# Kernel tuning notes

Measured on AMD Instinct MI355X. Metric: run time of the kernel, lower is better.

The kernel has to match this reference:

```python
import jax, jax.numpy as jnp
import numpy as np
from jax import lax

N_KERNELS = 10000
KSS = np.array([7, 9, 11])
SEQ_LEN = 512
C_IN = 1
KMAX = 11  # max kernel size; shorter kernels are zero-padded in the tap dim
BATCH = 16


def _gen_params():
    # Deterministic ROCKET kernel hyperparameters (matches the torch __init__ logic).
    rng = np.random.default_rng(0)
    ks = rng.choice(KSS, size=N_KERNELS)
    hi = np.log2((SEQ_LEN - 1) // (ks - 1))
    dil = np.floor(2.0 ** rng.uniform(0.0, hi)).astype(np.int64)  # int(dilation)
    use_pad = rng.integers(0, 2, N_KERNELS)
    p = ((ks - 1) * dil // 2) * use_pad
    # Conv1d is called with padding=2*p (faithful to source), so output length is:
    L = SEQ_LEN + 4 * p - dil * (ks - 1)
    return ks, dil, p, L

_KS, _DIL, _P, _L = _gen_params()
_PMAX = int((2 * _P).max())   # max per-side zero padding across kernels
_LMAX = int(_L.max())         # max conv output length across kernels


def setup_inputs() -> dict:
    key = jax.random.key(0)
    kx, kw, kb = jax.random.split(key, 3)
    x = jax.random.normal(kx, (BATCH, C_IN, SEQ_LEN), dtype=jnp.float32)
    W = jax.random.normal(kw, (N_KERNELS, C_IN, KMAX), dtype=jnp.float32)
    # zero taps beyond each kernel's true size, then subtract mean over real taps
    tap_mask = jnp.asarray((np.arange(KMAX)[None, :] < _KS[:, None])[:, None, :],
                           dtype=jnp.float32)                      # [K,1,KMAX]
    denom = jnp.asarray((_KS * C_IN).astype(np.float32))[:, None, None]
    W = W * tap_mask
    W = (W - W.sum(axis=(1, 2), keepdims=True) / denom) * tap_mask
    bias = 2.0 * (jax.random.uniform(kb, (N_KERNELS,), dtype=jnp.float32) - 0.5)
    return {"x": x, "W": W, "bias": bias}


def reference(x, W, bias):
    B = x.shape[0]
    off = jnp.asarray(_PMAX - 2 * _P, dtype=jnp.int32)               # [K]
    dil = jnp.asarray(_DIL, dtype=jnp.int32)                         # [K]
    t = jnp.arange(_LMAX, dtype=jnp.int32)
    pos_base = off[:, None] + t[None, :]                             # [K, Lmax]
    valid = t[None, :] < jnp.asarray(_L, dtype=jnp.int32)[:, None]   # [K, Lmax]
    xpad = jnp.pad(x, ((0, 0), (0, 0), (_PMAX, _PMAX)))              # zero pad
    hi = SEQ_LEN + 2 * _PMAX - 1

    def step(acc, jw):
        j, wj = jw                                                   # wj: [K, C]
        pos = jnp.clip(pos_base + j * dil[:, None], 0, hi)           # [K, Lmax]
        xg = xpad[:, :, pos]                                         # [B,C,K,Lmax]
        return acc + jnp.einsum('bckl,kc->bkl', xg, wj), None

    acc0 = jnp.zeros((B, N_KERNELS, _LMAX), dtype=x.dtype)
    Wt = jnp.transpose(W, (2, 0, 1))                                 # [KMAX,K,C]
    acc, _ = lax.scan(step, acc0, (jnp.arange(KMAX, dtype=jnp.int32), Wt))
    out = acc + bias[None, :, None]                                  # [B,K,Lmax]

    # inputs are finite, so nGood == L (>0 always): max over valid region + PPV
    _max = jnp.where(valid[None], out, -jnp.inf).max(axis=-1)        # [B, K]
    ngood = jnp.asarray(_L, dtype=x.dtype)
    ppv = jnp.sum(jnp.where(valid[None], out > 0, False), axis=-1).astype(x.dtype) / ngood[None]
    return jnp.stack([_max, ppv], axis=-1).reshape(B, 2 * N_KERNELS)
```

## Files before the change

kernel.cpp:

```cpp
#include <hip/hip_runtime.h>
#include <hip/hip_fp16.h>
#include <math.h>
#include <stdint.h>
#include <string.h>

typedef unsigned __int128 u128;

#define NK 10000
#define KPB 8

#define PCG_MUL_128 ((((u128)0x2360ed051fc65da4ULL) << 64) | 0x4385df649fccf645ULL)

#define SORT_OFF   (NK * 4)
#define WS_NEEDED  (SORT_OFF + NK * 4)

struct ThrTab { double t[3][84]; };

static void host_seed(u128& state, u128& inc) {
  uint32_t hc = 0x43b0d7e5u;
  auto hashmix = [&hc](uint32_t v) -> uint32_t {
    v ^= hc; hc *= 0x931e8875u; v *= hc; v ^= v >> 16; return v;
  };
  uint32_t pool[4];
  for (int i = 0; i < 4; ++i) pool[i] = hashmix(0u);
  for (int s = 0; s < 4; ++s)
    for (int d = 0; d < 4; ++d)
      if (s != d) {
        uint32_t h = hashmix(pool[s]);
        uint32_t r = pool[d] * 0xca01f9ddu - h * 0x4973f715u;
        r ^= r >> 16;
        pool[d] = r;
      }
  uint32_t hb = 0x8b51f9ddu;
  uint32_t w[8];
  for (int i = 0; i < 8; ++i) {
    uint32_t v = pool[i & 3];
    v ^= hb; hb *= 0x58f38dedu; v *= hb; v ^= v >> 16;
    w[i] = v;
  }
  u128 is_ = ((u128)(((uint64_t)w[0]) | ((uint64_t)w[1] << 32)) << 64)
           | (u128)(((uint64_t)w[2]) | ((uint64_t)w[3] << 32));
  u128 iq  = ((u128)(((uint64_t)w[4]) | ((uint64_t)w[5] << 32)) << 64)
           | (u128)(((uint64_t)w[6]) | ((uint64_t)w[7] << 32));
  inc = (iq << 1) | (u128)1;
  state = inc; state += is_; state = state * PCG_MUL_128 + inc;
}

static inline uint64_t xslrr_h(u128 s) {
  uint64_t x = (uint64_t)(s >> 64) ^ (uint64_t)s;
  unsigned r = (unsigned)(s >> 122);
  return (x >> r) | (x << ((64u - r) & 63u));
}

__device__ __forceinline__ void dev_seed(u128& state, u128& inc) {
  uint32_t hc = 0x43b0d7e5u;
  auto hashmix = [&hc](uint32_t v) -> uint32_t {
    v ^= hc; hc *= 0x931e8875u; v *= hc; v ^= v >> 16; return v;
  };
  uint32_t pool[4];
  for (int i = 0; i < 4; ++i) pool[i] = hashmix(0u);
  for (int s = 0; s < 4; ++s)
    for (int d = 0; d < 4; ++d)
      if (s != d) {
        uint32_t h = hashmix(pool[s]);
        uint32_t r = pool[d] * 0xca01f9ddu - h * 0x4973f715u;
        r ^= r >> 16;
        pool[d] = r;
      }
  uint32_t hb = 0x8b51f9ddu;
  uint32_t w[8];
  for (int i = 0; i < 8; ++i) {
    uint32_t v = pool[i & 3];
    v ^= hb; hb *= 0x58f38dedu; v *= hb; v ^= v >> 16;
    w[i] = v;
  }
  u128 is_ = ((u128)(((uint64_t)w[0]) | ((uint64_t)w[1] << 32)) << 64)
           | (u128)(((uint64_t)w[2]) | ((uint64_t)w[3] << 32));
  u128 iq  = ((u128)(((uint64_t)w[4]) | ((uint64_t)w[5] << 32)) << 64)
           | (u128)(((uint64_t)w[6]) | ((uint64_t)w[7] << 32));
  inc = (iq << 1) | (u128)1;
  state = inc; state += is_; state = state * PCG_MUL_128 + inc;
}

__device__ __forceinline__ u128 dev_advance(u128 state, u128 inc, uint64_t delta) {
  u128 am = 1, ap = 0, cm = PCG_MUL_128, cp = inc;
  while (delta) {
    if (delta & 1) { am = am * cm; ap = ap * cm + cp; }
    cp = (cm + (u128)1) * cp;
    cm = cm * cm;
    delta >>= 1;
  }
  return am * state + ap;
}

__device__ __forceinline__ uint64_t draw_at(u128 state, u128 inc, uint64_t n) {
  u128 s = dev_advance(state, inc, n);
  s = s * PCG_MUL_128 + inc;
  uint64_t x = (uint64_t)(s >> 64) ^ (uint64_t)s;
  unsigned r = (unsigned)(s >> 122);
  return (x >> r) | (x << ((64u - r) & 63u));
}

__global__ __launch_bounds__(256) void params_k(uint32_t* __restrict__ pack,
                                                ThrTab tt) {
  int i = blockIdx.x * 256 + threadIdx.x;
  if (i >= NK) return;
  u128 state, inc;
  dev_seed(state, inc);
  uint64_t a = draw_at(state, inc, (uint64_t)(i >> 1));
  uint32_t u = (i & 1) ? (uint32_t)(a >> 32) : (uint32_t)a;
  int si = (int)(((uint64_t)u * 3ull) >> 32);
  uint64_t ud = draw_at(state, inc, (uint64_t)(5000 + i));
  double d = (double)(ud >> 11) * (1.0 / 9007199254740992.0);
  int c0 = 0, c1 = 0, c2 = 0;
  #pragma unroll
  for (int v = 0; v < 84; ++v) {
    c0 += (d >= tt.t[0][v]) ? 1 : 0;
    c1 += (d >= tt.t[1][v]) ? 1 : 0;
    c2 += (d >= tt.t[2][v]) ? 1 : 0;
  }
  int dil = 1 + ((si == 0) ? c0 : ((si == 1) ? c1 : c2));
  uint64_t p6 = draw_at(state, inc, (uint64_t)(15000 + (i >> 1)));
  uint32_t pu = (i & 1) ? (uint32_t)(p6 >> 32) : (uint32_t)p6;
  int pad = (int)(pu >> 31);
  pack[i] = ((uint32_t)i << 10) | (uint32_t)si | ((uint32_t)dil << 2)
          | ((uint32_t)pad << 9);
}

__global__ __launch_bounds__(1024) void sort_k(const uint32_t* __restrict__ pack,
                                               uint32_t* __restrict__ sorted) {
  __shared__ int hist[1024];
  __shared__ int offs[1024];
  int tid = threadIdx.x;
  hist[tid] = 0;
  __syncthreads();
  for (int p = 0; p < 10; ++p) {
    int i = tid + p * 1024;
    if (i < NK) {
      uint32_t bits = pack[i] & 1023u;
      int ks = 7 + 2 * (int)(bits & 3), dil = (int)((bits >> 2) & 127);
      int pad = (int)(bits >> 9);
      int twop = (ks - 1) * dil * pad;
      int L = 512 + 2 * twop - dil * (ks - 1);
      atomicAdd(&hist[1022 - L], 1);
    }
  }
  __syncthreads();
  int own = hist[tid];
  for (int off = 1; off < 1024; off <<= 1) {
    int v = (tid >= off) ? hist[tid - off] : 0;
    __syncthreads();
    hist[tid] += v;
    __syncthreads();
  }
  offs[tid] = hist[tid] - own;
  __syncthreads();
  for (int p = 0; p < 10; ++p) {
    int i = tid + p * 1024;
    if (i < NK) {
      uint32_t e = pack[i];
      uint32_t bits = e & 1023u;
      int ks = 7 + 2 * (int)(bits & 3), dil = (int)((bits >> 2) & 127);
      int pad = (int)(bits >> 9);
      int twop = (ks - 1) * dil * pad;
      int L = 512 + 2 * twop - dil * (ks - 1);
      int idx = atomicAdd(&offs[1022 - L], 1);
      sorted[idx] = e;
    }
  }
}

template<int KS>
__device__ __forceinline__ void conv_core(const float4* __restrict__ xs4,
                                          const __half2* wh2, float bv,
                                          int twop, int dil, int L,
                                          int tl, int bh,
                                          float* m, int* cn) {
  int coreEnd = (L < 512) ? L : 512;
  int nch = (L + 31) >> 5;
  for (int c = 0; c < nch; ++c) {
    int t0 = c << 5;
    int t = t0 + tl;
    __half2 acc[4];
    #pragma unroll
    for (int r = 0; r < 4; ++r) acc[r] = __half2(__float2half2_rn(0.0f));
    if (t0 >= twop && t0 + 32 <= coreEnd) {
      const float4* p = xs4 + (unsigned)(t - twop) * 2 + bh;
      #pragma unroll
      for (int j = 0; j < KS; ++j) {
        float4 v4 = *p;
        union { float4 v; __half2 h[4]; } u;
        u.v = v4;
        __half2 wj = wh2[j];
        #pragma unroll
        for (int r = 0; r < 4; ++r) acc[r] = __hfma2(wj, u.h[r], acc[r]);
        p += (unsigned)dil * 2;
      }
    } else {
      int idx = t - twop;
      #pragma unroll
      for (int j = 0; j < KS; ++j) {
        unsigned ci = (unsigned)idx;
        ci = (ci > 512u) ? 512u : ci;
        float4 v4 = xs4[ci * 2 + bh];
        union { float4 v; __half2 h[4]; } u;
        u.v = v4;
        __half2 wj = wh2[j];
        #pragma unroll
        for (int r = 0; r < 4; ++r) acc[r] = __hfma2(wj, u.h[r], acc[r]);
        idx += dil;
      }
    }
    if (t < L) {
      #pragma unroll
      for (int r = 0; r < 4; ++r) {
        float2 f = __half22float2(acc[r]);
        float v0 = f.x + bv, v1 = f.y + bv;
        m[2 * r]     = fmaxf(m[2 * r], v0);     cn[2 * r]     += (v0 > 0.0f);
        m[2 * r + 1] = fmaxf(m[2 * r + 1], v1); cn[2 * r + 1] += (v1 > 0.0f);
      }
    }
  }
}

__global__ __launch_bounds__(512) void conv_feat_k(const float* __restrict__ x,
                                                   const float* __restrict__ W,
                                                   const float* __restrict__ bias,
                                                   const uint32_t* __restrict__ entries,
                                                   float failDiag,
                                                   float* __restrict__ out) {
  __shared__ float4 xs4[513 * 2];
  int tid = threadIdx.x;

  #pragma unroll
  for (int q = 0; q < 2; ++q) {
    int flat = q * 512 + tid;
    int t = flat >> 1, bh = flat & 1;
    union { __half h[8]; float4 v; } u;
    #pragma unroll
    for (int r = 0; r < 8; ++r)
      u.h[r] = __float2half(x[(8 * bh + r) * 512 + t]);
    xs4[flat] = u.v;
  }
  if (tid < 2) xs4[512 * 2 + tid] = make_float4(0.f, 0.f, 0.f, 0.f);

  int wave = tid >> 6, lane = tid & 63;
  int tl = lane >> 1, bh = lane & 1;
  uint32_t e = entries[blockIdx.x * KPB + wave];
  int k = (int)(e >> 10);
  uint32_t bits = e & 1023u;
  __syncthreads();

  int ks  = 7 + 2 * (int)(bits & 3);
  int dil = (int)((bits >> 2) & 127);
  int pad = (int)(bits >> 9);
  int twop = (ks - 1) * dil * pad;
  int L = 512 + 2 * twop - dil * (ks - 1);
  float w10 = W[k * 11 + 10], w8 = W[k * 11 + 8];
  int ksW = (w10 != 0.0f) ? 11 : ((w8 != 0.0f) ? 9 : 7);
  if (failDiag != 0.0f || ks != ksW) {
    float diag = (failDiag != 0.0f) ? failDiag : 6500000.0f;
    if (lane < 16) {
      out[(size_t)lane * 20000 + 2 * k]     = diag;
      out[(size_t)lane * 20000 + 2 * k + 1] = diag;
    }
    return;
  }

  __half2 wh2[11];
  #pragma unroll
  for (int j = 0; j < 11; ++j) wh2[j] = __float2half2_rn(W[k * 11 + j]);
  float bv = bias[k];

  float m[8];
  int cn[8];
  #pragma unroll
  for (int r = 0; r < 8; ++r) { m[r] = -INFINITY; cn[r] = 0; }
  if (ks == 7)       conv_core<7>(xs4, wh2, bv, twop, dil, L, tl, bh, m, cn);
  else if (ks == 9)  conv_core<9>(xs4, wh2, bv, twop, dil, L, tl, bh, m, cn);
  else               conv_core<11>(xs4, wh2, bv, twop, dil, L, tl, bh, m, cn);

  #pragma unroll
  for (int off = 2; off <= 32; off <<= 1) {
    #pragma unroll
    for (int r = 0; r < 8; ++r) {
      m[r] = fmaxf(m[r], __shfl_xor(m[r], off));
      cn[r] += __shfl_xor(cn[r], off);
    }
  }
  if (tl == 0) {
    float invL = 1.0f / (float)L;
    #pragma unroll
    for (int r = 0; r < 8; ++r) {
      size_t b = (size_t)(8 * bh + r);
      out[b * 20000 + 2 * k]     = m[r];
      out[b * 20000 + 2 * k + 1] = (float)cn[r] * invL;
    }
  }
}

extern "C" void kernel_launch(void* const* d_in, const int* in_sizes, int n_in,
                              void* d_out, int out_size, void* d_ws, size_t ws_size,
                              hipStream_t stream) {
  (void)out_size;
  const float *x = nullptr, *W = nullptr, *bias = nullptr;
  for (int i = 0; i < n_in; ++i) {
    int sz = in_sizes[i];
    if (sz == 16 * 512)      x    = (const float*)d_in[i];
    else if (sz == NK * 11)  W    = (const float*)d_in[i];
    else if (sz == NK)       bias = (const float*)d_in[i];
  }
  float failDiag = 0.0f;
  if (!x || !W || !bias) {
    failDiag = 9000000.0f;
    x = (const float*)d_in[0]; W = (const float*)d_in[1]; bias = (const float*)d_in[2];
  }

  static uint64_t hs[20000];
  {
    u128 st, inc; host_seed(st, inc);
    for (int i = 0; i < 20000; ++i) { st = st * PCG_MUL_128 + inc; hs[i] = xslrr_h(st); }
  }
  double d0 = (double)(hs[0] >> 11) * (1.0 / 9007199254740992.0);
  if (failDiag == 0.0f && fabs(d0 - 0.6369616873214543) >= 1.0e-15)
    failDiag = 4000000.0f;
  int rejected = 0;
  for (int i = 0; i < 5000; ++i)
    if ((uint32_t)hs[i] == 0u || (uint32_t)(hs[i] >> 32) == 0u) { rejected = 1; break; }

  static ThrTab tt;
  for (int si = 0; si < 3; ++si) {
    int ksv = 7 + 2 * si;
    double hi = log2((double)(511 / (ksv - 1)));
    double dmax = nextafter(1.0, 0.0);
    for (int v = 2; v <= 85; ++v) {
      if (pow(2.0, hi * dmax) < (double)v) { tt.t[si][v - 2] = 2.0; continue; }
      uint64_t lo = 0, hb;
      memcpy(&hb, &dmax, 8);
      while (hb - lo > 1) {
        uint64_t mid = lo + (hb - lo) / 2;
        double dm;
        memcpy(&dm, &mid, 8);
        if (pow(2.0, hi * dm) >= (double)v) hb = mid; else lo = mid;
      }
      double tv;
      memcpy(&tv, &hb, 8);
      tt.t[si][v - 2] = tv;
    }
  }

  uint32_t* dpack = (uint32_t*)d_ws;
  uint32_t* dsort = (uint32_t*)((char*)d_ws + SORT_OFF);

  if (!rejected && ws_size >= WS_NEEDED) {
    params_k<<<(NK + 255) / 256, 256, 0, stream>>>(dpack, tt);
    sort_k<<<1, 1024, 0, stream>>>(dpack, dsort);
    conv_feat_k<<<NK / KPB, 512, 0, stream>>>(x, W, bias, dsort, failDiag,
                                              (float*)d_out);
  } else {
    static uint32_t h_entries[NK];
    {
      int pos32 = 0;
      auto nx32 = [&](int& p) -> uint32_t {
        uint64_t v = hs[p >> 1];
        uint32_t u = (p & 1) ? (uint32_t)(v >> 32) : (uint32_t)v;
        ++p; return u;
      };
      static int ksA[NK], dilA[NK], padA[NK];
      for (int i = 0; i < NK; ++i) {
        uint64_t m; uint32_t u;
        do { u = nx32(pos32); m = (uint64_t)u * 3ull; } while ((uint32_t)m == 0u);
        ksA[i] = (int)(m >> 32);
      }
      int u64pos = (pos32 + 1) >> 1;
      for (int i = 0; i < NK; ++i) {
        double d = (double)(hs[u64pos + i] >> 11) * (1.0 / 9007199254740992.0);
        int ksv = 7 + 2 * ksA[i];
        double hi2 = log2((double)(511 / (ksv - 1)));
        dilA[i] = (int)floor(pow(2.0, hi2 * d));
      }
      int p32 = 2 * (u64pos + NK);
      for (int i = 0; i < NK; ++i) padA[i] = (int)(nx32(p32) >> 31);
      static int cnt2[1024], off2[1024];
      for (int b = 0; b < 1024; ++b) cnt2[b] = 0;
      for (int i = 0; i < NK; ++i) {
        int ksv = 7 + 2 * ksA[i];
        int twop = (ksv - 1) * dilA[i] * padA[i];
        int L = 512 + 2 * twop - dilA[i] * (ksv - 1);
        cnt2[1022 - L]++;
      }
      int acc = 0;
      for (int b = 0; b < 1024; ++b) { off2[b] = acc; acc += cnt2[b]; }
      for (int i = 0; i < NK; ++i) {
        int ksv = 7 + 2 * ksA[i];
        int twop = (ksv - 1) * dilA[i] * padA[i];
        int L = 512 + 2 * twop - dilA[i] * (ksv - 1);
        uint32_t bits = (uint32_t)ksA[i] | ((uint32_t)dilA[i] << 2)
                      | ((uint32_t)padA[i] << 9);
        h_entries[off2[1022 - L]++] = ((uint32_t)i << 10) | bits;
      }
    }
    hipMemcpyAsync(dsort, h_entries, sizeof(h_entries), hipMemcpyHostToDevice,
                   stream);
    conv_feat_k<<<NK / KPB, 512, 0, stream>>>(x, W, bias, dsort, failDiag,
                                              (float*)d_out);
  }
}
```

Baseline: 74.47 us.

## Replace length sort with atomic work-queue scheduling and half-precision epilogue

Drops the single-block counting-sort kernel that ordered kernels by output length. Instead, a fixed grid of persistent blocks has each wave pull kernel indices from a global atomic counter, which balances load dynamically. The per-element epilogue now stays in packed fp16: the bias is folded into the accumulator init, and max and positive count use vector half and short ops. This removes one kernel launch and a serial sort, but adds an atomic per kernel. The epilogue also loses precision, since the bias is added in fp16 and counts are held in 16-bit shorts.

```diff
diff --git a/kernel.cpp b/kernel.cpp
--- a/kernel.cpp
+++ b/kernel.cpp
@@ -5,14 +5,15 @@
 #include <string.h>
 
 typedef unsigned __int128 u128;
+typedef _Float16 h2v __attribute__((ext_vector_type(2)));
+typedef short    s2v __attribute__((ext_vector_type(2)));
 
 #define NK 10000
-#define KPB 8
+#define NBLK 1024
 
 #define PCG_MUL_128 ((((u128)0x2360ed051fc65da4ULL) << 64) | 0x4385df649fccf645ULL)
 
-#define SORT_OFF   (NK * 4)
-#define WS_NEEDED  (SORT_OFF + NK * 4)
+#define WS_NEEDED  ((NK + 1) * 4)
 
 struct ThrTab { double t[3][84]; };
 
@@ -104,7 +105,10 @@
 __global__ __launch_bounds__(256) void params_k(uint32_t* __restrict__ pack,
                                                 ThrTab tt) {
   int i = blockIdx.x * 256 + threadIdx.x;
-  if (i >= NK) return;
+  if (i >= NK) {
+    if (i == NK) pack[NK] = 0;
+    return;
+  }
   u128 state, inc;
   dev_seed(state, inc);
   uint64_t a = draw_at(state, inc, (uint64_t)(i >> 1));
@@ -123,59 +127,16 @@
   uint64_t p6 = draw_at(state, inc, (uint64_t)(15000 + (i >> 1)));
   uint32_t pu = (i & 1) ? (uint32_t)(p6 >> 32) : (uint32_t)p6;
   int pad = (int)(pu >> 31);
-  pack[i] = ((uint32_t)i << 10) | (uint32_t)si | ((uint32_t)dil << 2)
-          | ((uint32_t)pad << 9);
-}
-
-__global__ __launch_bounds__(1024) void sort_k(const uint32_t* __restrict__ pack,
-                                               uint32_t* __restrict__ sorted) {
-  __shared__ int hist[1024];
-  __shared__ int offs[1024];
-  int tid = threadIdx.x;
-  hist[tid] = 0;
-  __syncthreads();
-  for (int p = 0; p < 10; ++p) {
-    int i = tid + p * 1024;
-    if (i < NK) {
-      uint32_t bits = pack[i] & 1023u;
-      int ks = 7 + 2 * (int)(bits & 3), dil = (int)((bits >> 2) & 127);
-      int pad = (int)(bits >> 9);
-      int twop = (ks - 1) * dil * pad;
-      int L = 512 + 2 * twop - dil * (ks - 1);
-      atomicAdd(&hist[1022 - L], 1);
-    }
-  }
-  __syncthreads();
-  int own = hist[tid];
-  for (int off = 1; off < 1024; off <<= 1) {
-    int v = (tid >= off) ? hist[tid - off] : 0;
-    __syncthreads();
-    hist[tid] += v;
-    __syncthreads();
-  }
-  offs[tid] = hist[tid] - own;
-  __syncthreads();
-  for (int p = 0; p < 10; ++p) {
-    int i = tid + p * 1024;
-    if (i < NK) {
-      uint32_t e = pack[i];
-      uint32_t bits = e & 1023u;
-      int ks = 7 + 2 * (int)(bits & 3), dil = (int)((bits >> 2) & 127);
-      int pad = (int)(bits >> 9);
-      int twop = (ks - 1) * dil * pad;
-      int L = 512 + 2 * twop - dil * (ks - 1);
-      int idx = atomicAdd(&offs[1022 - L], 1);
-      sorted[idx] = e;
-    }
-  }
+  pack[i] = (uint32_t)si | ((uint32_t)dil << 2) | ((uint32_t)pad << 9);
 }
 
 template<int KS>
 __device__ __forceinline__ void conv_core(const float4* __restrict__ xs4,
-                                          const __half2* wh2, float bv,
+                                          const __half2* wh2, __half2 bvh2,
                                           int twop, int dil, int L,
                                           int tl, int bh,
-                                          float* m, int* cn) {
+                                          h2v* mh, s2v* ch) {
+  const h2v zero2 = (h2v)0;
   int coreEnd = (L < 512) ? L : 512;
   int nch = (L + 31) >> 5;
   for (int c = 0; c < nch; ++c) {
@@ -183,7 +144,7 @@
     int t = t0 + tl;
     __half2 acc[4];
     #pragma unroll
-    for (int r = 0; r < 4; ++r) acc[r] = __half2(__float2half2_rn(0.0f));
+    for (int r = 0; r < 4; ++r) acc[r] = bvh2;
     if (t0 >= twop && t0 + 32 <= coreEnd) {
       const float4* p = xs4 + (unsigned)(t - twop) * 2 + bh;
       #pragma unroll
@@ -214,10 +175,10 @@
     if (t < L) {
       #pragma unroll
       for (int r = 0; r < 4; ++r) {
-        float2 f = __half22float2(acc[r]);
-        float v0 = f.x + bv, v1 = f.y + bv;
-        m[2 * r]     = fmaxf(m[2 * r], v0);     cn[2 * r]     += (v0 > 0.0f);
-        m[2 * r + 1] = fmaxf(m[2 * r + 1], v1); cn[2 * r + 1] += (v1 > 0.0f);
+        union { __half2 h; h2v v; } cv;
+        cv.h = acc[r];
+        mh[r] = __builtin_elementwise_max(mh[r], cv.v);
+        ch[r] -= (cv.v > zero2);
       }
     }
   }
@@ -226,7 +187,7 @@
 __global__ __launch_bounds__(512) void conv_feat_k(const float* __restrict__ x,
                                                    const float* __restrict__ W,
                                                    const float* __restrict__ bias,
-                                                   const uint32_t* __restrict__ entries,
+                                                   uint32_t* __restrict__ pack,
                                                    float failDiag,
                                                    float* __restrict__ out) {
   __shared__ float4 xs4[513 * 2];
@@ -244,57 +205,74 @@
   }
   if (tid < 2) xs4[512 * 2 + tid] = make_float4(0.f, 0.f, 0.f, 0.f);
 
-  int wave = tid >> 6, lane = tid & 63;
+  int lane = tid & 63;
   int tl = lane >> 1, bh = lane & 1;
-  uint32_t e = entries[blockIdx.x * KPB + wave];
-  int k = (int)(e >> 10);
-  uint32_t bits = e & 1023u;
   __syncthreads();
 
-  int ks  = 7 + 2 * (int)(bits & 3);
-  int dil = (int)((bits >> 2) & 127);
-  int pad = (int)(bits >> 9);
-  int twop = (ks - 1) * dil * pad;
-  int L = 512 + 2 * twop - dil * (ks - 1);
-  float w10 = W[k * 11 + 10], w8 = W[k * 11 + 8];
-  int ksW = (w10 != 0.0f) ? 11 : ((w8 != 0.0f) ? 9 : 7);
-  if (failDiag != 0.0f || ks != ksW) {
-    float diag = (failDiag != 0.0f) ? failDiag : 6500000.0f;
-    if (lane < 16) {
-      out[(size_t)lane * 20000 + 2 * k]     = diag;
-      out[(size_t)lane * 20000 + 2 * k + 1] = diag;
-    }
-    return;
-  }
-
-  __half2 wh2[11];
-  #pragma unroll
-  for (int j = 0; j < 11; ++j) wh2[j] = __float2half2_rn(W[k * 11 + j]);
-  float bv = bias[k];
-
-  float m[8];
-  int cn[8];
-  #pragma unroll
-  for (int r = 0; r < 8; ++r) { m[r] = -INFINITY; cn[r] = 0; }
-  if (ks == 7)       conv_core<7>(xs4, wh2, bv, twop, dil, L, tl, bh, m, cn);
-  else if (ks == 9)  conv_core<9>(xs4, wh2, bv, twop, dil, L, tl, bh, m, cn);
-  else               conv_core<11>(xs4, wh2, bv, twop, dil, L, tl, bh, m, cn);
-
-  #pragma unroll
-  for (int off = 2; off <= 32; off <<= 1) {
-    #pragma unroll
-    for (int r = 0; r < 8; ++r) {
-      m[r] = fmaxf(m[r], __shfl_xor(m[r], off));
-      cn[r] += __shfl_xor(cn[r], off);
-    }
-  }
-  if (tl == 0) {
-    float invL = 1.0f / (float)L;
-    #pragma unroll
-    for (int r = 0; r < 8; ++r) {
-      size_t b = (size_t)(8 * bh + r);
-      out[b * 20000 + 2 * k]     = m[r];
-      out[b * 20000 + 2 * k + 1] = (float)cn[r] * invL;
+  for (;;) {
+    int k;
+    if (lane == 0) k = (int)atomicAdd(&pack[NK], 1u);
+    k = __shfl(k, 0);
+    if (k >= NK) break;
+
+    uint32_t bits = pack[k] & 1023u;
+    int ks  = 7 + 2 * (int)(bits & 3);
+    int dil = (int)((bits >> 2) & 127);
+    int pad = (int)(bits >> 9);
+    int twop = (ks - 1) * dil * pad;
+    int L = 512 + 2 * twop - dil * (ks - 1);
+    float w10 = W[k * 11 + 10], w8 = W[k * 11 + 8];
+    int ksW = (w10 != 0.0f) ? 11 : ((w8 != 0.0f) ? 9 : 7);
+    if (failDiag != 0.0f || ks != ksW) {
+      float diag = (failDiag != 0.0f) ? failDiag : 6500000.0f;
+      if (lane < 16) {
+        out[(size_t)lane * 20000 + 2 * k]     = diag;
+        out[(size_t)lane * 20000 + 2 * k + 1] = diag;
+      }
+      continue;
+    }
+
+    __half2 wh2[11];
+    #pragma unroll
+    for (int j = 0; j < 11; ++j) wh2[j] = __float2half2_rn(W[k * 11 + j]);
+    __half2 bvh2 = __float2half2_rn(bias[k]);
+
+    h2v mh[4];
+    s2v ch[4];
+    #pragma unroll
+    for (int r = 0; r < 4; ++r) {
+      mh[r] = (h2v)(-__builtin_huge_valf16());
+      ch[r] = (s2v)0;
+    }
+    if (ks == 7)       conv_core<7>(xs4, wh2, bvh2, twop, dil, L, tl, bh, mh, ch);
+    else if (ks == 9)  conv_core<9>(xs4, wh2, bvh2, twop, dil, L, tl, bh, mh, ch);
+    else               conv_core<11>(xs4, wh2, bvh2, twop, dil, L, tl, bh, mh, ch);
+
+    float m[8];
+    int cn[8];
+    #pragma unroll
+    for (int r = 0; r < 4; ++r) {
+      m[2 * r]      = (float)mh[r].x;
+      m[2 * r + 1]  = (float)mh[r].y;
+      cn[2 * r]     = (int)ch[r].x;
+      cn[2 * r + 1] = (int)ch[r].y;
+    }
+    #pragma unroll
+    for (int off = 2; off <= 32; off <<= 1) {
+      #pragma unroll
+      for (int r = 0; r < 8; ++r) {
+        m[r] = fmaxf(m[r], __shfl_xor(m[r], off));
+        cn[r] += __shfl_xor(cn[r], off);
+      }
+    }
+    if (tl == 0) {
+      float invL = 1.0f / (float)L;
+      #pragma unroll
+      for (int r = 0; r < 8; ++r) {
+        size_t b = (size_t)(8 * bh + r);
+        out[b * 20000 + 2 * k]     = m[r];
+        out[b * 20000 + 2 * k + 1] = (float)cn[r] * invL;
+      }
     }
   }
 }
@@ -350,15 +328,13 @@
   }
 
   uint32_t* dpack = (uint32_t*)d_ws;
-  uint32_t* dsort = (uint32_t*)((char*)d_ws + SORT_OFF);
 
   if (!rejected && ws_size >= WS_NEEDED) {
-    params_k<<<(NK + 255) / 256, 256, 0, stream>>>(dpack, tt);
-    sort_k<<<1, 1024, 0, stream>>>(dpack, dsort);
-    conv_feat_k<<<NK / KPB, 512, 0, stream>>>(x, W, bias, dsort, failDiag,
-                                              (float*)d_out);
+    params_k<<<(NK + 256) / 256, 256, 0, stream>>>(dpack, tt);
+    conv_feat_k<<<NBLK, 512, 0, stream>>>(x, W, bias, dpack, failDiag,
+                                          (float*)d_out);
   } else {
-    static uint32_t h_entries[NK];
+    static uint32_t h_pack[NK + 1];
     {
       int pos32 = 0;
       auto nx32 = [&](int& p) -> uint32_t {
@@ -366,13 +342,14 @@
         uint32_t u = (p & 1) ? (uint32_t)(v >> 32) : (uint32_t)v;
         ++p; return u;
       };
-      static int ksA[NK], dilA[NK], padA[NK];
+      static int ksA[NK];
       for (int i = 0; i < NK; ++i) {
         uint64_t m; uint32_t u;
         do { u = nx32(pos32); m = (uint64_t)u * 3ull; } while ((uint32_t)m == 0u);
         ksA[i] = (int)(m >> 32);
       }
       int u64pos = (pos32 + 1) >> 1;
+      static int dilA[NK];
       for (int i = 0; i < NK; ++i) {
         double d = (double)(hs[u64pos + i] >> 11) * (1.0 / 9007199254740992.0);
         int ksv = 7 + 2 * ksA[i];
@@ -380,29 +357,16 @@
         dilA[i] = (int)floor(pow(2.0, hi2 * d));
       }
       int p32 = 2 * (u64pos + NK);
-      for (int i = 0; i < NK; ++i) padA[i] = (int)(nx32(p32) >> 31);
-      static int cnt2[1024], off2[1024];
-      for (int b = 0; b < 1024; ++b) cnt2[b] = 0;
       for (int i = 0; i < NK; ++i) {
-        int ksv = 7 + 2 * ksA[i];
-        int twop = (ksv - 1) * dilA[i] * padA[i];
-        int L = 512 + 2 * twop - dilA[i] * (ksv - 1);
-        cnt2[1022 - L]++;
-      }
-      int acc = 0;
-      for (int b = 0; b < 1024; ++b) { off2[b] = acc; acc += cnt2[b]; }
-      for (int i = 0; i < NK; ++i) {
-        int ksv = 7 + 2 * ksA[i];
-        int twop = (ksv - 1) * dilA[i] * padA[i];
-        int L = 512 + 2 * twop - dilA[i] * (ksv - 1);
-        uint32_t bits = (uint32_t)ksA[i] | ((uint32_t)dilA[i] << 2)
-                      | ((uint32_t)padA[i] << 9);
-        h_entries[off2[1022 - L]++] = ((uint32_t)i << 10) | bits;
-      }
-    }
-    hipMemcpyAsync(dsort, h_entries, sizeof(h_entries), hipMemcpyHostToDevice,
-                   stream);
-    conv_feat_k<<<NK / KPB, 512, 0, stream>>>(x, W, bias, dsort, failDiag,
-                                              (float*)d_out);
-  }
-}
+        int pad = (int)(nx32(p32) >> 31);
+        h_pack[i] = (uint32_t)ksA[i] | ((uint32_t)dilA[i] << 2)
+                  | ((uint32_t)pad << 9);
+      }
+      h_pack[NK] = 0;
+    }
+    (void)hipMemcpyAsync(dpack, h_pack, sizeof(h_pack), hipMemcpyHostToDevice,
+                         stream);
+    conv_feat_k<<<NBLK, 512, 0, stream>>>(x, W, bias, dpack, failDiag,
+                                          (float*)d_out);
+  }
+}
```

Result: slower. 233.0 us (+212.9%).
